# Optimization experiments

Hardware: AMD Instinct MI355X
Metric: run time of the kernel (lower is better)

The kernel has to match this reference:

```python
import jax, jax.numpy as jnp
import numpy as np

H = 64  # hidden_size
F = 32  # input_size
B, T = 4096, 256


def setup_inputs() -> dict:
    key = jax.random.key(0)
    ks = jax.random.split(key, 12)
    s = 1.0 / np.sqrt(H)  # torch LSTM init scale
    u = lambda k, shape: jax.random.uniform(k, shape, jnp.float32, -s, s)
    return {
        "x": jax.random.normal(ks[0], (B, T, F), jnp.float32),
        # layer 0 (input_size=F)
        "W_ih0": u(ks[1], (4 * H, F)),
        "W_hh0": u(ks[2], (4 * H, H)),
        "b_ih0": u(ks[3], (4 * H,)),
        "b_hh0": u(ks[4], (4 * H,)),
        # layer 1 (input_size=H)
        "W_ih1": u(ks[5], (4 * H, H)),
        "W_hh1": u(ks[6], (4 * H, H)),
        "b_ih1": u(ks[7], (4 * H,)),
        "b_hh1": u(ks[8], (4 * H,)),
        # linear head
        "W_out": u(ks[9], (1, H)),
        "b_out": u(ks[10], (1,)),
    }


def _lstm_layer(x, W_ih, W_hh, b_ih, b_hh):
    # x: [B, T, D] -> hidden sequence [B, T, H]; PyTorch gate order i,f,g,o.
    b = x.shape[0]
    h_dim = W_hh.shape[1]
    # precompute input contribution for all timesteps: [B, T, 4H]
    gx = jnp.einsum('btd,gd->btg', x, W_ih) + b_ih + b_hh

    def step(carry, g_t):
        h, c = carry
        g = g_t + h @ W_hh.T  # [B, 4H]
        i, f, gg, o = jnp.split(g, 4, axis=-1)
        c = jax.nn.sigmoid(f) * c + jax.nn.sigmoid(i) * jnp.tanh(gg)
        h = jax.nn.sigmoid(o) * jnp.tanh(c)
        return (h, c), h

    h0 = jnp.zeros((b, h_dim), x.dtype)
    (_, _), hs = jax.lax.scan(step, (h0, h0), jnp.swapaxes(gx, 0, 1))
    return jnp.swapaxes(hs, 0, 1)  # [B, T, H]


def reference(x, W_ih0, W_hh0, b_ih0, b_hh0, W_ih1, W_hh1, b_ih1, b_hh1, W_out, b_out):
    h = _lstm_layer(x, W_ih0, W_hh0, b_ih0, b_hh0)
    h = _lstm_layer(h, W_ih1, W_hh1, b_ih1, b_hh1)
    last = h[:, -1, :]  # [B, H]; dropout is identity at inference
    return last @ W_out.T + b_out  # [B, 1]
```

## Files before the change

kernel.cpp:

```cpp
#include <hip/hip_runtime.h>

typedef _Float16 half8 __attribute__((ext_vector_type(8)));
typedef _Float16 half4 __attribute__((ext_vector_type(4)));
typedef _Float16 half2_t __attribute__((ext_vector_type(2)));
typedef float f32x4 __attribute__((ext_vector_type(4)));

#define T_STEPS 256
#define NB      16
#define NBLOCKS (4096/NB)
#define LOG2E   1.4426950408889634f

#define S1 104
#define S2 152

__device__ __forceinline__ unsigned int pack2(float a, float b) {
    half2_t h;
    h.x = (_Float16)a;
    h.y = (_Float16)b;
    return __builtin_bit_cast(unsigned int, h);
}

__device__ __forceinline__ half8 cvt8s(const float* __restrict__ p) {
    half8 r;
    #pragma unroll
    for (int j = 0; j < 8; ++j) r[j] = (_Float16)(p[j] * LOG2E);
    return r;
}

__device__ __forceinline__ void sync_lds() {
    asm volatile("s_waitcnt lgkmcnt(0)" ::: "memory");
    __builtin_amdgcn_s_barrier();
}

__global__ __launch_bounds__(512, 1)
void lstm_pipe8(const float* __restrict__ x,
                const float* __restrict__ Wih0, const float* __restrict__ Whh0,
                const float* __restrict__ bih0, const float* __restrict__ bhh0,
                const float* __restrict__ Wih1, const float* __restrict__ Whh1,
                const float* __restrict__ bih1, const float* __restrict__ bhh1,
                const float* __restrict__ Wout, const float* __restrict__ bout,
                float* __restrict__ out)
{
    __shared__ _Float16 A1[2][16][S1];
    __shared__ _Float16 A2[2][16][S2];

    const int tid  = threadIdx.x;
    const int w    = tid >> 6;
    const bool isL1 = (w < 4);
    const int wq   = w & 3;
    const int l    = tid & 63;
    const int ln   = l & 15;
    const int lb   = l >> 4;
    const int ub   = 16 * wq + 4 * lb;
    const int gb0  = blockIdx.x * NB;

    half8 wa[4][4];
    f32x4 bv[4];
    if (isL1) {
        #pragma unroll
        for (int q = 0; q < 4; ++q) {
            const int g = 64 * q + 16 * wq + ln;
            #pragma unroll
            for (int ks = 0; ks < 3; ++ks) {
                const int c0 = 32 * ks + 8 * lb;
                const float* p = (c0 < 32) ? (Wih0 + g * 32 + c0)
                                           : (Whh0 + g * 64 + (c0 - 32));
                wa[q][ks] = cvt8s(p);
            }
            #pragma unroll
            for (int jj = 0; jj < 4; ++jj) {
                const int gj = 64 * q + ub + jj;
                bv[q][jj] = (bih0[gj] + bhh0[gj]) * LOG2E;
            }
        }
    } else {
        #pragma unroll
        for (int q = 0; q < 4; ++q) {
            const int g = 64 * q + 16 * wq + ln;
            #pragma unroll
            for (int ks = 0; ks < 4; ++ks) {
                const int c0 = 32 * ks + 8 * lb;
                const float* p = (c0 < 64) ? (Wih1 + g * 64 + c0)
                                           : (Whh1 + g * 64 + (c0 - 64));
                wa[q][ks] = cvt8s(p);
            }
            #pragma unroll
            for (int jj = 0; jj < 4; ++jj) {
                const int gj = 64 * q + ub + jj;
                bv[q][jj] = (bih1[gj] + bhh1[gj]) * LOG2E;
            }
        }
    }

    float cst[4] = {0.f, 0.f, 0.f, 0.f};

    {
        unsigned int* z = (unsigned int*)A1;
        for (int i = tid; i < (int)(sizeof(A1) / 4); i += 512) z[i] = 0u;
        unsigned int* z2 = (unsigned int*)A2;
        for (int i = tid; i < (int)(sizeof(A2) / 4); i += 512) z2[i] = 0u;
    }
    sync_lds();

    const int sbx = tid >> 4, sdx = tid & 15;
    const float* xbase = x + (long)(gb0 + sbx) * T_STEPS * 32 + 2 * sdx;
    float2 xva = {0.f, 0.f}, xvb = {0.f, 0.f};
    if (isL1) {
        const float2 x0 = *(const float2*)xbase;
        *(unsigned int*)&A1[0][sbx][2 * sdx] = pack2(x0.x, x0.y);
        xva = *(const float2*)(xbase + 32);
        xvb = *(const float2*)(xbase + 64);
    }
    sync_lds();

#define ACT(JJ)                                                                \
    {                                                                          \
        const float si = acc[0][JJ], sf = acc[1][JJ];                          \
        const float sg = acc[2][JJ], so = acc[3][JJ];                          \
        const float ei = __builtin_amdgcn_exp2f(-si);                          \
        const float ef = __builtin_amdgcn_exp2f(-sf);                          \
        const float Eg = __builtin_amdgcn_exp2f(sg + sg);                      \
        const float eo = __builtin_amdgcn_exp2f(-so);                          \
        const float ti = 1.f + ei, tf = 1.f + ef, tg = 1.f + Eg;               \
        const float pig = ti * tg;                                             \
        const float num = cst[JJ] * pig + (Eg - 1.f) * tf;                     \
        const float c   = num * __builtin_amdgcn_rcpf(pig * tf);               \
        cst[JJ] = c;                                                           \
        const float Ec  = __builtin_amdgcn_exp2f(fminf((2.f * LOG2E) * c, 120.f)); \
        hh[JJ] = (_Float16)((Ec - 1.f) *                                       \
                 __builtin_amdgcn_rcpf((1.f + eo) * (1.f + Ec)));              \
    }

#define STEP(J, P)                                                             \
    do {                                                                       \
        if (isL1 && (J) < T_STEPS) {                                           \
                \
            if ((J) < T_STEPS - 1)                                             \
                *(unsigned int*)&A1[1 - (P)][sbx][2 * sdx] = pack2(xva.x, xva.y); \
            xva = xvb;                                                         \
            if ((J) + 3 < T_STEPS) xvb = *(const float2*)(xbase + ((J) + 3) * 32); \
                                   \
            const half8 bf0 = *(const half8*)&A1[P][ln][8 * lb];               \
            const half8 bf1 = *(const half8*)&A1[P][ln][32 + 8 * lb];          \
            const half8 bf2 = *(const half8*)&A1[P][ln][64 + 8 * lb];          \
            f32x4 acc[4];                                                      \
            _Pragma("unroll")                                                  \
            for (int q = 0; q < 4; ++q) {                                      \
                acc[q] = bv[q];                                                \
                acc[q] = __builtin_amdgcn_mfma_f32_16x16x32_f16(wa[q][0], bf0, acc[q], 0, 0, 0); \
                acc[q] = __builtin_amdgcn_mfma_f32_16x16x32_f16(wa[q][1], bf1, acc[q], 0, 0, 0); \
                acc[q] = __builtin_amdgcn_mfma_f32_16x16x32_f16(wa[q][2], bf2, acc[q], 0, 0, 0); \
            }                                                                  \
            half4 hh;                                                          \
            ACT(0) ACT(1) ACT(2) ACT(3)                                        \
            *(half4*)&A1[1 - (P)][ln][32 + ub] = hh;                           \
            *(half4*)&A2[1 - (P)][ln][ub] = hh;                                \
        }                                                                      \
        if (!isL1 && (J) > 0) {                                                \
             \
            const half8 bf0 = *(const half8*)&A2[P][ln][8 * lb];               \
            const half8 bf1 = *(const half8*)&A2[P][ln][32 + 8 * lb];          \
            const half8 bf2 = *(const half8*)&A2[P][ln][64 + 8 * lb];          \
            const half8 bf3 = *(const half8*)&A2[P][ln][96 + 8 * lb];          \
            f32x4 acc[4];                                                      \
            _Pragma("unroll")                                                  \
            for (int q = 0; q < 4; ++q) {                                      \
                acc[q] = bv[q];                                                \
                acc[q] = __builtin_amdgcn_mfma_f32_16x16x32_f16(wa[q][0], bf0, acc[q], 0, 0, 0); \
                acc[q] = __builtin_amdgcn_mfma_f32_16x16x32_f16(wa[q][1], bf1, acc[q], 0, 0, 0); \
                acc[q] = __builtin_amdgcn_mfma_f32_16x16x32_f16(wa[q][2], bf2, acc[q], 0, 0, 0); \
                acc[q] = __builtin_amdgcn_mfma_f32_16x16x32_f16(wa[q][3], bf3, acc[q], 0, 0, 0); \
            }                                                                  \
            half4 hh;                                                          \
            ACT(0) ACT(1) ACT(2) ACT(3)                                        \
            *(half4*)&A2[1 - (P)][ln][64 + ub] = hh;                           \
        }                                                                      \
        sync_lds();                                                            \
    } while (0)

    for (int jj = 0; jj < T_STEPS; jj += 2) {
        STEP(jj, 0);
        STEP(jj + 1, 1);
    }
    STEP(T_STEPS, 0);

    if (tid < NB) {
        float s = bout[0];
        #pragma unroll 8
        for (int u = 0; u < 64; ++u)
            s += (float)A2[1][tid][64 + u] * Wout[u];
        out[gb0 + tid] = s;
    }
}

extern "C" void kernel_launch(void* const* d_in, const int* in_sizes, int n_in,
                              void* d_out, int out_size, void* d_ws, size_t ws_size,
                              hipStream_t stream) {
    const float* x    = (const float*)d_in[0];
    const float* Wih0 = (const float*)d_in[1];
    const float* Whh0 = (const float*)d_in[2];
    const float* bih0 = (const float*)d_in[3];
    const float* bhh0 = (const float*)d_in[4];
    const float* Wih1 = (const float*)d_in[5];
    const float* Whh1 = (const float*)d_in[6];
    const float* bih1 = (const float*)d_in[7];
    const float* bhh1 = (const float*)d_in[8];
    const float* Wout = (const float*)d_in[9];
    const float* bout = (const float*)d_in[10];

    hipLaunchKernelGGL(lstm_pipe8, dim3(NBLOCKS), dim3(512), 0, stream,
                       x, Wih0, Whh0, bih0, bhh0,
                       Wih1, Whh1, bih1, bhh1, Wout, bout,
                       (float*)d_out);
}
```

Baseline: 184.9 us.

## Precompute next-step input projection in registers and merge LDS hidden buffers

Layer-1 waves now compute the x·W_ih projection for the next timestep directly from registers loaded from global memory, one step ahead, off the recurrent critical path. x is no longer staged through LDS, and one MFMA per gate drops out of the dependent chain. Gate pre-activation scales (negation, doubling for tanh) are folded into the fp16 weights and biases, and the two LDS buffers are merged into one shared hidden buffer. s_setprio is raised around the MFMA blocks. The change adds register pressure and per-step global loads inside the loop.

```diff
diff --git a/kernel.cpp b/kernel.cpp
--- a/kernel.cpp
+++ b/kernel.cpp
@@ -2,7 +2,6 @@
 
 typedef _Float16 half8 __attribute__((ext_vector_type(8)));
 typedef _Float16 half4 __attribute__((ext_vector_type(4)));
-typedef _Float16 half2_t __attribute__((ext_vector_type(2)));
 typedef float f32x4 __attribute__((ext_vector_type(4)));
 
 #define T_STEPS 256
@@ -10,20 +9,12 @@
 #define NBLOCKS (4096/NB)
 #define LOG2E   1.4426950408889634f
 
-#define S1 104
-#define S2 152
-
-__device__ __forceinline__ unsigned int pack2(float a, float b) {
-    half2_t h;
-    h.x = (_Float16)a;
-    h.y = (_Float16)b;
-    return __builtin_bit_cast(unsigned int, h);
-}
-
-__device__ __forceinline__ half8 cvt8s(const float* __restrict__ p) {
+#define SH 136
+
+__device__ __forceinline__ half8 cvt8s(const float* __restrict__ p, float s) {
     half8 r;
     #pragma unroll
-    for (int j = 0; j < 8; ++j) r[j] = (_Float16)(p[j] * LOG2E);
+    for (int j = 0; j < 8; ++j) r[j] = (_Float16)(p[j] * s);
     return r;
 }
 
@@ -33,16 +24,15 @@
 }
 
 __global__ __launch_bounds__(512, 1)
-void lstm_pipe8(const float* __restrict__ x,
-                const float* __restrict__ Wih0, const float* __restrict__ Whh0,
-                const float* __restrict__ bih0, const float* __restrict__ bhh0,
-                const float* __restrict__ Wih1, const float* __restrict__ Whh1,
-                const float* __restrict__ bih1, const float* __restrict__ bhh1,
-                const float* __restrict__ Wout, const float* __restrict__ bout,
-                float* __restrict__ out)
+void lstm_v5(const float* __restrict__ x,
+             const float* __restrict__ Wih0, const float* __restrict__ Whh0,
+             const float* __restrict__ bih0, const float* __restrict__ bhh0,
+             const float* __restrict__ Wih1, const float* __restrict__ Whh1,
+             const float* __restrict__ bih1, const float* __restrict__ bhh1,
+             const float* __restrict__ Wout, const float* __restrict__ bout,
+             float* __restrict__ out)
 {
-    __shared__ _Float16 A1[2][16][S1];
-    __shared__ _Float16 A2[2][16][S2];
+    __shared__ _Float16 Hb[2][16][SH];
 
     const int tid  = threadIdx.x;
     const int w    = tid >> 6;
@@ -55,39 +45,39 @@
     const int gb0  = blockIdx.x * NB;
 
     half8 wa[4][4];
+    half8 wax[4];
     f32x4 bv[4];
     if (isL1) {
         #pragma unroll
         for (int q = 0; q < 4; ++q) {
+            const float s = (q == 2) ? 2.f * LOG2E : -LOG2E;
             const int g = 64 * q + 16 * wq + ln;
-            #pragma unroll
-            for (int ks = 0; ks < 3; ++ks) {
-                const int c0 = 32 * ks + 8 * lb;
-                const float* p = (c0 < 32) ? (Wih0 + g * 32 + c0)
-                                           : (Whh0 + g * 64 + (c0 - 32));
-                wa[q][ks] = cvt8s(p);
-            }
+            wax[q] = cvt8s(Wih0 + g * 32 + 8 * lb, s);
+            #pragma unroll
+            for (int ks = 0; ks < 2; ++ks)
+                wa[q][ks] = cvt8s(Whh0 + g * 64 + 32 * ks + 8 * lb, s);
             #pragma unroll
             for (int jj = 0; jj < 4; ++jj) {
                 const int gj = 64 * q + ub + jj;
-                bv[q][jj] = (bih0[gj] + bhh0[gj]) * LOG2E;
+                bv[q][jj] = (bih0[gj] + bhh0[gj]) * s;
             }
         }
     } else {
         #pragma unroll
         for (int q = 0; q < 4; ++q) {
+            const float s = (q == 2) ? 2.f * LOG2E : -LOG2E;
             const int g = 64 * q + 16 * wq + ln;
             #pragma unroll
             for (int ks = 0; ks < 4; ++ks) {
                 const int c0 = 32 * ks + 8 * lb;
                 const float* p = (c0 < 64) ? (Wih1 + g * 64 + c0)
                                            : (Whh1 + g * 64 + (c0 - 64));
-                wa[q][ks] = cvt8s(p);
+                wa[q][ks] = cvt8s(p, s);
             }
             #pragma unroll
             for (int jj = 0; jj < 4; ++jj) {
                 const int gj = 64 * q + ub + jj;
-                bv[q][jj] = (bih1[gj] + bhh1[gj]) * LOG2E;
+                bv[q][jj] = (bih1[gj] + bhh1[gj]) * s;
             }
         }
     }
@@ -95,35 +85,38 @@
     float cst[4] = {0.f, 0.f, 0.f, 0.f};
 
     {
-        unsigned int* z = (unsigned int*)A1;
-        for (int i = tid; i < (int)(sizeof(A1) / 4); i += 512) z[i] = 0u;
-        unsigned int* z2 = (unsigned int*)A2;
-        for (int i = tid; i < (int)(sizeof(A2) / 4); i += 512) z2[i] = 0u;
+        unsigned int* z = (unsigned int*)Hb;
+        for (int i = tid; i < (int)(sizeof(Hb) / 4); i += 512) z[i] = 0u;
+    }
+
+    const float* xb = x + (long)(gb0 + ln) * T_STEPS * 32 + 8 * lb;
+    f32x4 xr0 = {0.f,0.f,0.f,0.f}, xr1 = {0.f,0.f,0.f,0.f};
+    f32x4 gxA[4], gxB[4];
+    if (isL1) {
+        xr0 = *(const f32x4*)(xb);
+        xr1 = *(const f32x4*)(xb + 4);
+        half8 xf;
+        #pragma unroll
+        for (int j = 0; j < 4; ++j) { xf[j] = (_Float16)xr0[j]; xf[4+j] = (_Float16)xr1[j]; }
+        #pragma unroll
+        for (int q = 0; q < 4; ++q) {
+            gxA[q] = bv[q];
+            gxA[q] = __builtin_amdgcn_mfma_f32_16x16x32_f16(wax[q], xf, gxA[q], 0, 0, 0);
+        }
+        xr0 = *(const f32x4*)(xb + 32);
+        xr1 = *(const f32x4*)(xb + 36);
     }
     sync_lds();
 
-    const int sbx = tid >> 4, sdx = tid & 15;
-    const float* xbase = x + (long)(gb0 + sbx) * T_STEPS * 32 + 2 * sdx;
-    float2 xva = {0.f, 0.f}, xvb = {0.f, 0.f};
-    if (isL1) {
-        const float2 x0 = *(const float2*)xbase;
-        *(unsigned int*)&A1[0][sbx][2 * sdx] = pack2(x0.x, x0.y);
-        xva = *(const float2*)(xbase + 32);
-        xvb = *(const float2*)(xbase + 64);
-    }
-    sync_lds();
-
-#define ACT(JJ)                                                                \
+#define ACT1(A, JJ)                                                            \
     {                                                                          \
-        const float si = acc[0][JJ], sf = acc[1][JJ];                          \
-        const float sg = acc[2][JJ], so = acc[3][JJ];                          \
-        const float ei = __builtin_amdgcn_exp2f(-si);                          \
-        const float ef = __builtin_amdgcn_exp2f(-sf);                          \
-        const float Eg = __builtin_amdgcn_exp2f(sg + sg);                      \
-        const float eo = __builtin_amdgcn_exp2f(-so);                          \
+        const float ei = __builtin_amdgcn_exp2f(A[0][JJ]);                     \
+        const float ef = __builtin_amdgcn_exp2f(A[1][JJ]);                     \
+        const float Eg = __builtin_amdgcn_exp2f(A[2][JJ]);                     \
+        const float eo = __builtin_amdgcn_exp2f(A[3][JJ]);                     \
         const float ti = 1.f + ei, tf = 1.f + ef, tg = 1.f + Eg;               \
         const float pig = ti * tg;                                             \
-        const float num = cst[JJ] * pig + (Eg - 1.f) * tf;                     \
+        const float num = fmaf(Eg - 1.f, tf, cst[JJ] * pig);                   \
         const float c   = num * __builtin_amdgcn_rcpf(pig * tf);               \
         cst[JJ] = c;                                                           \
         const float Ec  = __builtin_amdgcn_exp2f(fminf((2.f * LOG2E) * c, 120.f)); \
@@ -131,64 +124,76 @@
                  __builtin_amdgcn_rcpf((1.f + eo) * (1.f + Ec)));              \
     }
 
-#define STEP(J, P)                                                             \
+#define STEP(J, P, GXC, GXN)                                                   \
     do {                                                                       \
         if (isL1 && (J) < T_STEPS) {                                           \
-                \
-            if ((J) < T_STEPS - 1)                                             \
-                *(unsigned int*)&A1[1 - (P)][sbx][2 * sdx] = pack2(xva.x, xva.y); \
-            xva = xvb;                                                         \
-            if ((J) + 3 < T_STEPS) xvb = *(const float2*)(xbase + ((J) + 3) * 32); \
-                                   \
-            const half8 bf0 = *(const half8*)&A1[P][ln][8 * lb];               \
-            const half8 bf1 = *(const half8*)&A1[P][ln][32 + 8 * lb];          \
-            const half8 bf2 = *(const half8*)&A1[P][ln][64 + 8 * lb];          \
-            f32x4 acc[4];                                                      \
+                                                \
+            const half8 bf0 = *(const half8*)&Hb[P][ln][8 * lb];               \
+            const half8 bf1 = *(const half8*)&Hb[P][ln][32 + 8 * lb];          \
+                         \
+            half8 xf;                                                          \
+            _Pragma("unroll")                                                  \
+            for (int j = 0; j < 4; ++j) { xf[j] = (_Float16)xr0[j]; xf[4+j] = (_Float16)xr1[j]; } \
+            _Pragma("unroll")                                                  \
+            for (int q = 0; q < 4; ++q) GXN[q] = bv[q];                        \
+            _Pragma("unroll")                                                  \
+            for (int q = 0; q < 4; ++q)                                        \
+                GXN[q] = __builtin_amdgcn_mfma_f32_16x16x32_f16(wax[q], xf, GXN[q], 0, 0, 0); \
+                          \
+            { const int jn = ((J) + 2 < T_STEPS) ? (J) + 2 : T_STEPS - 1;      \
+              xr0 = *(const f32x4*)(xb + jn * 32);                             \
+              xr1 = *(const f32x4*)(xb + jn * 32 + 4); }                       \
+                                                   \
+            __builtin_amdgcn_s_setprio(1);                                     \
             _Pragma("unroll")                                                  \
             for (int q = 0; q < 4; ++q) {                                      \
-                acc[q] = bv[q];                                                \
-                acc[q] = __builtin_amdgcn_mfma_f32_16x16x32_f16(wa[q][0], bf0, acc[q], 0, 0, 0); \
-                acc[q] = __builtin_amdgcn_mfma_f32_16x16x32_f16(wa[q][1], bf1, acc[q], 0, 0, 0); \
-                acc[q] = __builtin_amdgcn_mfma_f32_16x16x32_f16(wa[q][2], bf2, acc[q], 0, 0, 0); \
+                GXC[q] = __builtin_amdgcn_mfma_f32_16x16x32_f16(wa[q][0], bf0, GXC[q], 0, 0, 0); \
+                GXC[q] = __builtin_amdgcn_mfma_f32_16x16x32_f16(wa[q][1], bf1, GXC[q], 0, 0, 0); \
             }                                                                  \
+            __builtin_amdgcn_s_setprio(0);                                     \
             half4 hh;                                                          \
-            ACT(0) ACT(1) ACT(2) ACT(3)                                        \
-            *(half4*)&A1[1 - (P)][ln][32 + ub] = hh;                           \
-            *(half4*)&A2[1 - (P)][ln][ub] = hh;                                \
+            ACT1(GXC, 0) ACT1(GXC, 1) ACT1(GXC, 2) ACT1(GXC, 3)                \
+            *(half4*)&Hb[1 - (P)][ln][ub] = hh;                                \
         }                                                                      \
         if (!isL1 && (J) > 0) {                                                \
-             \
-            const half8 bf0 = *(const half8*)&A2[P][ln][8 * lb];               \
-            const half8 bf1 = *(const half8*)&A2[P][ln][32 + 8 * lb];          \
-            const half8 bf2 = *(const half8*)&A2[P][ln][64 + 8 * lb];          \
-            const half8 bf3 = *(const half8*)&A2[P][ln][96 + 8 * lb];          \
+            const half8 bf0 = *(const half8*)&Hb[P][ln][8 * lb];               \
+            const half8 bf1 = *(const half8*)&Hb[P][ln][32 + 8 * lb];          \
+            const half8 bf2 = *(const half8*)&Hb[P][ln][64 + 8 * lb];          \
+            const half8 bf3 = *(const half8*)&Hb[P][ln][96 + 8 * lb];          \
             f32x4 acc[4];                                                      \
             _Pragma("unroll")                                                  \
+            for (int q = 0; q < 4; ++q) acc[q] = bv[q];                        \
+            __builtin_amdgcn_s_setprio(1);                                     \
+            _Pragma("unroll")                                                  \
             for (int q = 0; q < 4; ++q) {                                      \
-                acc[q] = bv[q];                                                \
                 acc[q] = __builtin_amdgcn_mfma_f32_16x16x32_f16(wa[q][0], bf0, acc[q], 0, 0, 0); \
                 acc[q] = __builtin_amdgcn_mfma_f32_16x16x32_f16(wa[q][1], bf1, acc[q], 0, 0, 0); \
                 acc[q] = __builtin_amdgcn_mfma_f32_16x16x32_f16(wa[q][2], bf2, acc[q], 0, 0, 0); \
                 acc[q] = __builtin_amdgcn_mfma_f32_16x16x32_f16(wa[q][3], bf3, acc[q], 0, 0, 0); \
             }                                                                  \
+            __builtin_amdgcn_s_setprio(0);                                     \
             half4 hh;                                                          \
-            ACT(0) ACT(1) ACT(2) ACT(3)                                        \
-            *(half4*)&A2[1 - (P)][ln][64 + ub] = hh;                           \
+            ACT1(acc, 0) ACT1(acc, 1) ACT1(acc, 2) ACT1(acc, 3)                \
+            *(half4*)&Hb[1 - (P)][ln][64 + ub] = hh;                           \
         }                                                                      \
         sync_lds();                                                            \
     } while (0)
 
     for (int jj = 0; jj < T_STEPS; jj += 2) {
-        STEP(jj, 0);
-        STEP(jj + 1, 1);
-    }
-    STEP(T_STEPS, 0);
+        STEP(jj, 0, gxA, gxB);
+        STEP(jj + 1, 1, gxB, gxA);
+    }
+    STEP(T_STEPS, 0, gxA, gxB);
 
     if (tid < NB) {
         float s = bout[0];
-        #pragma unroll 8
-        for (int u = 0; u < 64; ++u)
-            s += (float)A2[1][tid][64 + u] * Wout[u];
+        #pragma unroll
+        for (int u8 = 0; u8 < 8; ++u8) {
+            const half8 hv = *(const half8*)&Hb[1][tid][64 + 8 * u8];
+            #pragma unroll
+            for (int j = 0; j < 8; ++j)
+                s += (float)hv[j] * Wout[8 * u8 + j];
+        }
         out[gb0 + tid] = s;
     }
 }
@@ -208,7 +213,7 @@
     const float* Wout = (const float*)d_in[9];
     const float* bout = (const float*)d_in[10];
 
-    hipLaunchKernelGGL(lstm_pipe8, dim3(NBLOCKS), dim3(512), 0, stream,
+    hipLaunchKernelGGL(lstm_v5, dim3(NBLOCKS), dim3(512), 0, stream,
                        x, Wih0, Whh0, bih0, bhh0,
                        Wih1, Whh1, bih1, bhh1, Wout, bout,
                        (float*)d_out);
```

New measurement: 174.2 us. 1.06x faster.
